# Optimization experiments

Measured on AMD Instinct MI355X. Metric: run time of the kernel, lower is better.

Reference implementation:

```python
import jax, jax.numpy as jnp
import numpy as np

DIM = 768
NH = 12
HD = DIM // NH  # 64, also the depthwise-pool channel count
SR = 2
EPS_SRN = 1e-6   # sr_norm / up_norm eps
EPS_LN = 1e-5    # default nn.LayerNorm eps for norm_q/k/v


def ln(x, g, b, eps):
    m = x.mean(-1, keepdims=True)
    v = x.var(-1, keepdims=True)
    return (x - m) / jnp.sqrt(v + eps) * g + b


def dwconv(x, w, stride, pad, bias=None):
    # x [N,C,H,W], w [C*m,1,kh,kw] (torch depthwise layout), groups = C
    y = jax.lax.conv_general_dilated(
        x, w, (stride, stride), [(pad, pad), (pad, pad)],
        feature_group_count=x.shape[1],
        dimension_numbers=('NCHW', 'OIHW', 'NCHW'))
    return y if bias is None else y + bias[None, :, None, None]


def setup_inputs() -> dict:
    key = jax.random.key(0)
    ks = jax.random.split(key, 8)
    B, H, W = 8, 56, 56
    N = H * W
    s = 0.02
    f32 = jnp.float32
    d = {
        'x': jax.random.normal(ks[0], (B, N, DIM), f32),
        'q_w': jax.random.normal(ks[1], (DIM, DIM), f32) * s,
        'q_b': jnp.zeros((DIM,), f32),
        'kv_w': jax.random.normal(ks[2], (DIM, 2 * DIM), f32) * s,
        'kv_b': jnp.zeros((2 * DIM,), f32),
        'sr_w': jax.random.normal(ks[3], (DIM, 1, 3, 3), f32) * s,
        'sr_b': jnp.zeros((DIM,), f32),
        'srn_g': jnp.ones((DIM,), f32), 'srn_b': jnp.zeros((DIM,), f32),
        'up_w': jax.random.normal(ks[4], (SR * SR * DIM, 1, 3, 3), f32) * s,
        'up_b': jnp.zeros((SR * SR * DIM,), f32),
        'upn_g': jnp.ones((DIM,), f32), 'upn_b': jnp.zeros((DIM,), f32),
        'proj_w': jax.random.normal(ks[5], (DIM, DIM), f32) * s,
        'proj_b': jnp.zeros((DIM,), f32),
        'pq_w': jax.random.normal(ks[6], (HD, 1, 3, 3), f32) * s,
        'pk_w': jax.random.normal(ks[7], (HD, 1, 3, 3), f32) * s,
        'pv_w': jax.random.normal(jax.random.fold_in(key, 7), (HD, 1, 3, 3), f32) * s,
        'nq_g': jnp.ones((HD,), f32), 'nq_b': jnp.zeros((HD,), f32),
        'nk_g': jnp.ones((HD,), f32), 'nk_b': jnp.zeros((HD,), f32),
        'nv_g': jnp.ones((HD,), f32), 'nv_b': jnp.zeros((HD,), f32),
        'H': H, 'W': W,
    }
    return d


def _forward(x, q_w, q_b, kv_w, kv_b, sr_w, sr_b, srn_g, srn_b,
             up_w, up_b, upn_g, upn_b, proj_w, proj_b,
             pq_w, pk_w, pv_w, nq_g, nq_b, nk_g, nk_b, nv_g, nv_b, H, W):
    B, N, C = x.shape
    scale = HD ** -0.5
    # q projection -> [B, NH, N, HD]
    q = (x @ q_w + q_b).reshape(B, N, NH, HD).transpose(0, 2, 1, 3)
    # pool_q: per-head depthwise 3x3 stride-1 conv + LayerNorm(HD)
    qi = q.reshape(B * NH, H, W, HD).transpose(0, 3, 1, 2)
    qi = dwconv(qi, pq_w, 1, 1)
    q = qi.reshape(B, NH, HD, H * W).transpose(0, 1, 3, 2)
    q = ln(q, nq_g, nq_b, EPS_LN)
    # spatial reduction of x (depthwise k=3, s=2, p=1) + LayerNorm
    xs = x.transpose(0, 2, 1).reshape(B, C, H, W)
    xs = dwconv(xs, sr_w, SR, SR // 2, sr_b)
    Hs, Ws = xs.shape[2], xs.shape[3]  # H//SR, W//SR
    xs = xs.reshape(B, C, Hs * Ws).transpose(0, 2, 1)
    xs = ln(xs, srn_g, srn_b, EPS_SRN)
    # kv projection -> k, v [B, NH, Hs*Ws, HD]
    kv = (xs @ kv_w + kv_b).reshape(B, Hs * Ws, 2, NH, HD).transpose(2, 0, 3, 1, 4)
    k, v = kv[0], kv[1]

    def pool_kv(t, w, g, b):
        ti = t.reshape(B * NH, Hs, Ws, HD).transpose(0, 3, 1, 2)
        ti = dwconv(ti, w, 2, 1)  # stride_kv=(2,2), pad 1
        hk, wk = ti.shape[2], ti.shape[3]
        t2 = ti.reshape(B, NH, HD, hk * wk).transpose(0, 1, 3, 2)
        return ln(t2, g, b, EPS_LN)

    kp = pool_kv(k, pk_w, nk_g, nk_b)
    vp = pool_kv(v, pv_w, nv_g, nv_b)
    # attention core
    attn = jax.nn.softmax(jnp.einsum('bhnd,bhmd->bhnm', q, kp) * scale, axis=-1)
    out = jnp.einsum('bhnm,bhmd->bhnd', attn, vp).transpose(0, 2, 1, 3).reshape(B, N, C)
    # identity path: unpooled v -> depthwise conv -> PixelShuffle(SR) upsample
    idn = v.transpose(0, 1, 3, 2).reshape(B, C, Hs, Ws)
    idn = dwconv(idn, up_w, 1, 1, up_b)  # [B, SR*SR*C, Hs, Ws], groups=C
    idn = idn.reshape(B, C, SR, SR, Hs, Ws).transpose(0, 1, 4, 2, 5, 3).reshape(B, C, Hs * SR, Ws * SR)
    idn = idn.reshape(B, C, N).transpose(0, 2, 1)
    idn = ln(idn, upn_g, upn_b, EPS_SRN)
    return (out + idn) @ proj_w + proj_b


def reference(x, q_w, q_b, kv_w, kv_b, sr_w, sr_b, srn_g, srn_b,
              up_w, up_b, upn_g, upn_b, proj_w, proj_b,
              pq_w, pk_w, pv_w, nq_g, nq_b, nk_g, nk_b, nv_g, nv_b, H, W):
    return _forward(x, q_w, q_b, kv_w, kv_b, sr_w, sr_b, srn_g, srn_b,
                    up_w, up_b, upn_g, upn_b, proj_w, proj_b,
                    pq_w, pk_w, pv_w, nq_g, nq_b, nk_g, nk_b, nv_g, nv_b, H, W)
```

## Files before the change

### kernel.cpp

```cpp
#include <hip/hip_runtime.h>
#include <cstdint>
#include <cstddef>

#define DIM 768
#define NHD 12
#define HD  64
#define HH  56
#define WW  56
#define NQ  3136
#define HS  28
#define WSS 28
#define NS  784
#define HK  14
#define WK  14
#define NKK 196
#define NKP 224
#define VSTR 256
#define PROWB 512

typedef __bf16 bf16x8 __attribute__((ext_vector_type(8)));
typedef __bf16 bf16x4 __attribute__((ext_vector_type(4)));
typedef float  f32x4  __attribute__((ext_vector_type(4)));

__device__ __forceinline__ int xcd_swizzle(int bid, int nwg) {
  const int q = nwg >> 3, r = nwg & 7;
  const int xcd = bid & 7, off = bid >> 3;
  return (xcd < r ? xcd * (q + 1) : r * (q + 1) + (xcd - r) * q) + off;
}

__device__ __forceinline__ void gload_lds16(const void* g, void* l) {
  __builtin_amdgcn_global_load_lds(
      (const __attribute__((address_space(1))) void*)g,
      (__attribute__((address_space(3))) void*)l, 16, 0, 0);
}

#define LDP 48

template<int MODE>
__global__ __launch_bounds__(256) void gemm_mfma_kernel(
    const __bf16* __restrict__ A, const __bf16* __restrict__ Bt,
    const float* __restrict__ bias, float* __restrict__ C,
    __bf16* __restrict__ Cq, int M, int N, int K)
{
  __shared__ __bf16 As[128 * LDP];
  __shared__ __bf16 Bs[128 * LDP];

  const int nX = N >> 7;
  const int bid = xcd_swizzle(blockIdx.x, (M >> 7) * nX);
  const int row0 = (bid / nX) << 7;
  const int col0 = (bid % nX) << 7;

  const int t = threadIdx.x;
  const int lane = t & 63;
  const int w = t >> 6;
  const int wr = w >> 1, wc = w & 1;

  const int rs = t >> 1;
  const int kh = (t & 1) << 4;
  const __bf16* Aptr = A + (size_t)(row0 + rs) * K + kh;
  const __bf16* Bptr = Bt + (size_t)(col0 + rs) * K + kh;

  f32x4 acc[4][4];
#pragma unroll
  for (int i = 0; i < 4; ++i)
#pragma unroll
    for (int j = 0; j < 4; ++j) acc[i][j] = (f32x4){0.f, 0.f, 0.f, 0.f};

  const int fr = lane & 15;
  const int fc = lane >> 4;

  int4 a0 = *(const int4*)(Aptr);
  int4 a1 = *(const int4*)(Aptr + 8);
  int4 b0 = *(const int4*)(Bptr);
  int4 b1 = *(const int4*)(Bptr + 8);

  const int NT = K >> 5;
  for (int kt = 0; kt < NT; ++kt) {
    __syncthreads();
    *(int4*)(&As[rs * LDP + kh]) = a0;
    *(int4*)(&As[rs * LDP + kh + 8]) = a1;
    *(int4*)(&Bs[rs * LDP + kh]) = b0;
    *(int4*)(&Bs[rs * LDP + kh + 8]) = b1;
    __syncthreads();
    if (kt + 1 < NT) {
      const __bf16* ap = Aptr + ((kt + 1) << 5);
      const __bf16* bp = Bptr + ((kt + 1) << 5);
      a0 = *(const int4*)(ap);
      a1 = *(const int4*)(ap + 8);
      b0 = *(const int4*)(bp);
      b1 = *(const int4*)(bp + 8);
    }
    bf16x8 af[4], bfr[4];
#pragma unroll
    for (int i = 0; i < 4; ++i)
      af[i] = *(const bf16x8*)(&As[(wr * 64 + i * 16 + fr) * LDP + fc * 8]);
#pragma unroll
    for (int j = 0; j < 4; ++j)
      bfr[j] = *(const bf16x8*)(&Bs[(wc * 64 + j * 16 + fr) * LDP + fc * 8]);
#pragma unroll
    for (int i = 0; i < 4; ++i)
#pragma unroll
      for (int j = 0; j < 4; ++j)
        acc[i][j] = __builtin_amdgcn_mfma_f32_16x16x32_bf16(af[i], bfr[j], acc[i][j], 0, 0, 0);
  }

  const int orow = row0 + wr * 64 + ((lane >> 4) << 2);
  const int ocol = col0 + wc * 64 + (lane & 15);
#pragma unroll
  for (int j = 0; j < 4; ++j) {
    const int col = ocol + j * 16;
    const float bv = bias[col];
#pragma unroll
    for (int i = 0; i < 4; ++i)
#pragma unroll
      for (int r = 0; r < 4; ++r) {
        const int rrow = orow + i * 16 + r;
        if (MODE == 0) {
          C[(size_t)rrow * N + col] = acc[i][j][r] + bv;
        } else if (MODE == 1) {
          const int b = rrow / NQ, n = rrow - b * NQ;
          const int h = col >> 6, hd = col & 63;
          Cq[(((size_t)b * NHD + h) * NQ + n) * HD + hd] = (__bf16)(acc[i][j][r] + bv);
        } else {
          Cq[(size_t)rrow * N + col] = (__bf16)(acc[i][j][r] + bv);
        }
      }
  }
}

__global__ __launch_bounds__(256) void cast_bf16_kernel(
    const float* __restrict__ in, __bf16* __restrict__ out, long n4)
{
  long i = (long)blockIdx.x * 256 + threadIdx.x;
  const long stride = (long)gridDim.x * 256;
  for (; i < n4; i += stride) {
    float4 v = *(const float4*)(in + i * 4);
    bf16x4 o;
    o.x = (__bf16)v.x; o.y = (__bf16)v.y; o.z = (__bf16)v.z; o.w = (__bf16)v.w;
    *(bf16x4*)(out + i * 4) = o;
  }
}

__global__ __launch_bounds__(256) void wt_cast_kernel(
    const float* __restrict__ W, __bf16* __restrict__ Wt, int K, int N)
{
  __shared__ float tile[32][33];
  const int k0 = blockIdx.y << 5;
  const int n0 = blockIdx.x << 5;
  const int tc = threadIdx.x & 31;
  const int tr = threadIdx.x >> 5;
#pragma unroll
  for (int i = 0; i < 4; ++i)
    tile[tr + i * 8][tc] = W[(size_t)(k0 + tr + i * 8) * N + n0 + tc];
  __syncthreads();
#pragma unroll
  for (int i = 0; i < 4; ++i)
    Wt[(size_t)(n0 + tr + i * 8) * K + k0 + tc] = (__bf16)tile[tc][tr + i * 8];
}

__global__ __launch_bounds__(256) void up_tr_kernel(
    const float* __restrict__ upw, float* __restrict__ upt)
{
  const int i = blockIdx.x * 256 + threadIdx.x;
  if (i < 4 * 9 * DIM) {
    const int c = i % DIM;
    const int rest = i / DIM;
    const int tap = rest % 9, sidx = rest / 9;
    upt[i] = upw[(c * 4 + sidx) * 9 + tap];
  }
}

__global__ __launch_bounds__(256) void sr_tr_kernel(
    const float* __restrict__ srw, float* __restrict__ srt)
{
  const int i = blockIdx.x * 256 + threadIdx.x;
  if (i < 9 * DIM) {
    const int c = i % DIM;
    const int tap = i / DIM;
    srt[i] = srw[c * 9 + tap];
  }
}

__global__ __launch_bounds__(256) void pool_q_ln_kernel(
    const __bf16* __restrict__ qp, const float* __restrict__ pqw,
    const float* __restrict__ g, const float* __restrict__ bb,
    __bf16* __restrict__ qf)
{
  const int blk = xcd_swizzle(blockIdx.x, gridDim.x);
  const int bh = blk / HH, y = blk - bh * HH;
  const int lane = threadIdx.x & 63;
  const int w = threadIdx.x >> 6;
  const int x0 = w * (WW / 4);

  float wt[9];
#pragma unroll
  for (int tap = 0; tap < 9; ++tap) {
    const int yy = y - 1 + tap / 3;
    wt[tap] = (yy >= 0 && yy < HH) ? pqw[lane * 9 + tap] : 0.f;
  }
  const float gl = g[lane], bl = bb[lane];

  const __bf16* rp0;
  const __bf16* rp1;
  const __bf16* rp2;
  {
    const __bf16* base = qp + (size_t)bh * NQ * HD + lane;
    rp0 = base + (size_t)min(max(y - 1, 0), HH - 1) * WW * HD;
    rp1 = base + (size_t)y * WW * HD;
    rp2 = base + (size_t)min(max(y + 1, 0), HH - 1) * WW * HD;
  }
  auto ldc = [&](int xx, float* d) {
    const float m = (xx >= 0 && xx < WW) ? 1.f : 0.f;
    const int xc = min(max(xx, 0), WW - 1);
    d[0] = m * (float)rp0[(size_t)xc * HD];
    d[1] = m * (float)rp1[(size_t)xc * HD];
    d[2] = m * (float)rp2[(size_t)xc * HD];
  };

  float c0[3], c1[3], c2[3], cn[3];
  ldc(x0 - 1, c0);
  ldc(x0,     c1);
  ldc(x0 + 1, c2);

#pragma unroll
  for (int xi = 0; xi < WW / 4; ++xi) {
    const int x = x0 + xi;
    ldc(x + 2, cn);
    float acc = 0.f;
#pragma unroll
    for (int dy = 0; dy < 3; ++dy) {
      acc = fmaf(wt[dy * 3 + 0], c0[dy], acc);
      acc = fmaf(wt[dy * 3 + 1], c1[dy], acc);
      acc = fmaf(wt[dy * 3 + 2], c2[dy], acc);
    }
    float s = acc, sq = acc * acc;
#pragma unroll
    for (int off = 32; off > 0; off >>= 1) {
      s  += __shfl_xor(s, off);
      sq += __shfl_xor(sq, off);
    }
    const float mean = s * (1.f / 64.f);
    const float var  = sq * (1.f / 64.f) - mean * mean;
    const float rstd = rsqrtf(var + 1e-5f);
    qf[((size_t)bh * NQ + y * WW + x) * HD + lane] =
        (__bf16)((acc - mean) * rstd * gl + bl);
#pragma unroll
    for (int dy = 0; dy < 3; ++dy) {
      c0[dy] = c1[dy]; c1[dy] = c2[dy]; c2[dy] = cn[dy];
    }
  }
}

__global__ __launch_bounds__(256) void sr_ln_kernel(
    const __bf16* __restrict__ x, const float* __restrict__ srt,
    const float* __restrict__ srb, const float* __restrict__ g,
    const float* __restrict__ bb, __bf16* __restrict__ out)
{
  const int row = xcd_swizzle(blockIdx.x, gridDim.x);
  const int b = row / NS, ns = row - b * NS;
  const int ys = ns / WSS, xs = ns - ys * WSS;
  const int t = threadIdx.x;

  float fm[9];
  size_t off9[9];
#pragma unroll
  for (int tap = 0; tap < 9; ++tap) {
    const int yy = 2 * ys - 1 + tap / 3;
    const int xx = 2 * xs - 1 + tap % 3;
    fm[tap] = (yy >= 0 && yy < HH && xx >= 0 && xx < WW) ? 1.f : 0.f;
    const int yyc = min(max(yy, 0), HH - 1);
    const int xxc = min(max(xx, 0), WW - 1);
    off9[tap] = ((size_t)b * NQ + yyc * WW + xxc) * DIM;
  }

  float vals[3];
  float lsum = 0.f, lsq = 0.f;
#pragma unroll
  for (int i = 0; i < 3; ++i) {
    const int c = t + i * 256;
    float v9[9];
#pragma unroll
    for (int tap = 0; tap < 9; ++tap) v9[tap] = (float)x[off9[tap] + c];
    float acc = srb[c];
#pragma unroll
    for (int tap = 0; tap < 9; ++tap)
      acc = fmaf(srt[tap * DIM + c] * fm[tap], v9[tap], acc);
    vals[i] = acc;
    lsum += acc;
    lsq = fmaf(acc, acc, lsq);
  }
#pragma unroll
  for (int off = 32; off > 0; off >>= 1) {
    lsum += __shfl_xor(lsum, off);
    lsq  += __shfl_xor(lsq, off);
  }
  __shared__ float s1[4], s2[4];
  if ((t & 63) == 0) { s1[t >> 6] = lsum; s2[t >> 6] = lsq; }
  __syncthreads();
  const float S  = s1[0] + s1[1] + s1[2] + s1[3];
  const float SQ = s2[0] + s2[1] + s2[2] + s2[3];
  const float mean = S * (1.f / 768.f);
  const float var  = SQ * (1.f / 768.f) - mean * mean;
  const float rstd = rsqrtf(var + 1e-6f);
#pragma unroll
  for (int i = 0; i < 3; ++i) {
    const int c = t + i * 256;
    out[(size_t)row * DIM + c] = (__bf16)((vals[i] - mean) * rstd * g[c] + bb[c]);
  }
}

__global__ __launch_bounds__(256) void pool_kv_ln_kernel(
    const __bf16* __restrict__ kv, const float* __restrict__ pkw,
    const float* __restrict__ pvw, const float* __restrict__ kg,
    const float* __restrict__ kbb, const float* __restrict__ vg,
    const float* __restrict__ vbb, __bf16* __restrict__ kpb,
    __bf16* __restrict__ vtb)
{
  const int isv = blockIdx.y;
  const float* pw = isv ? pvw : pkw;
  const float* g  = isv ? vg  : kg;
  const float* bb = isv ? vbb : kbb;
  const int coloff = isv ? DIM : 0;

  const int lane = threadIdx.x & 63;
  const int r = blockIdx.x * 4 + (threadIdx.x >> 6);
  const int bh = r / NKP;
  const int nk = r - bh * NKP;

  float val = 0.f;
  if (nk < NKK) {
    const int b = bh / NHD, h = bh - b * NHD;
    const int yk = nk / WK, xk = nk - yk * WK;
    float acc = 0.f;
#pragma unroll
    for (int dy = 0; dy < 3; ++dy) {
      const int yy = 2 * yk - 1 + dy;
      if (yy < 0 || yy >= HS) continue;
#pragma unroll
      for (int dx = 0; dx < 3; ++dx) {
        const int xx = 2 * xk - 1 + dx;
        if (xx < 0 || xx >= WSS) continue;
        acc = fmaf(pw[lane * 9 + dy * 3 + dx],
                   (float)kv[((size_t)b * NS + yy * WSS + xx) * (2 * DIM) + coloff + h * HD + lane], acc);
      }
    }
    float s = acc, sq = acc * acc;
#pragma unroll
    for (int off = 32; off > 0; off >>= 1) {
      s  += __shfl_xor(s, off);
      sq += __shfl_xor(sq, off);
    }
    const float mean = s * (1.f / 64.f);
    const float var  = sq * (1.f / 64.f) - mean * mean;
    const float rstd = rsqrtf(var + 1e-5f);
    val = (acc - mean) * rstd * g[lane] + bb[lane];
  }
  if (!isv) {
    kpb[(size_t)bh * NKP * HD + nk * HD + (lane ^ ((nk & 7) << 3))] = (__bf16)val;
  } else {
    vtb[(size_t)bh * HD * VSTR + lane * VSTR + (nk ^ ((lane & 7) << 3))] = (__bf16)val;
  }
}

__global__ __launch_bounds__(256) void attn_mfma_kernel(
    const __bf16* __restrict__ qf, const __bf16* __restrict__ kpb,
    const __bf16* __restrict__ vtb, __bf16* __restrict__ out)
{
  __shared__ __bf16 kp_lds[16384];
  __shared__ __bf16 v_lds[16384];
  const int bh = blockIdx.y;
  const int qt = blockIdx.x;
  const int t = threadIdx.x;
  const int lane = t & 63, w = t >> 6;
  const int fr = lane & 15;
  const int fg = lane >> 4;
  const int q0 = qt * 64 + w * 16;
  const int sw = (fr & 7) << 4;

  const __bf16* qbase = qf + ((size_t)bh * NQ + q0) * HD;
  const bf16x8 aq0 = *(const bf16x8*)(qbase + fr * HD + fg * 8);
  const bf16x8 aq1 = *(const bf16x8*)(qbase + fr * HD + 32 + fg * 8);

  {
    const __bf16* kgp = kpb + (size_t)bh * (NKP * HD);
    const __bf16* vgp = vtb + (size_t)bh * (HD * VSTR);
    char* kl = (char*)kp_lds;
    char* vl = (char*)v_lds;
#pragma unroll
    for (int i = 0; i < 7; ++i)
      gload_lds16(kgp + (i * 256 + w * 64 + lane) * 8, kl + i * 4096 + w * 1024);
#pragma unroll
    for (int i = 0; i < 8; ++i)
      gload_lds16(vgp + (i * 256 + w * 64 + lane) * 8, vl + i * 4096 + w * 1024);
  }
  __syncthreads();

  const char* kl = (const char*)kp_lds;
  f32x4 s[13];
#pragma unroll
  for (int n = 0; n < 13; ++n) {
    const int rowb = (n * 16 + fr) << 7;
    const bf16x8 b0 = *(const bf16x8*)(kl + rowb + ((fg << 4) ^ sw));
    const bf16x8 b1 = *(const bf16x8*)(kl + rowb + (((fg << 4) + 64) ^ sw));
    f32x4 c = (f32x4){0.f, 0.f, 0.f, 0.f};
    c = __builtin_amdgcn_mfma_f32_16x16x32_bf16(b0, aq0, c, 0, 0, 0);
    c = __builtin_amdgcn_mfma_f32_16x16x32_bf16(b1, aq1, c, 0, 0, 0);
    s[n] = c;
  }
  __syncthreads();

  const float scale = 0.125f;
  char* pb = (char*)kp_lds;
  const int rbase = (w * 16 + fr) * PROWB;
  float sum = 0.f;
#pragma unroll
  for (int n = 0; n < 13; ++n) {
    float e0 = __expf(s[n][0] * scale);
    float e1 = __expf(s[n][1] * scale);
    float e2 = __expf(s[n][2] * scale);
    float e3 = __expf(s[n][3] * scale);
    if (n == 12 && fg >= 1) { e0 = e1 = e2 = e3 = 0.f; }
    sum += (e0 + e1) + (e2 + e3);
    bf16x4 pk4;
    pk4[0] = (__bf16)e0; pk4[1] = (__bf16)e1;
    pk4[2] = (__bf16)e2; pk4[3] = (__bf16)e3;
    *(bf16x4*)(pb + rbase + ((n * 32 + fg * 8) ^ sw)) = pk4;
  }
  {
    bf16x4 z; z[0] = z[1] = z[2] = z[3] = (__bf16)0.f;
    *(bf16x4*)(pb + rbase + ((13 * 32 + fg * 8) ^ sw)) = z;
  }
  sum += __shfl_xor(sum, 16);
  sum += __shfl_xor(sum, 32);
  const float pinvL = 1.f / sum;

  f32x4 acc2[4];
#pragma unroll
  for (int dt = 0; dt < 4; ++dt) acc2[dt] = (f32x4){0.f, 0.f, 0.f, 0.f};
  const char* vl = (const char*)v_lds;
#pragma unroll
  for (int ks = 0; ks < 7; ++ks) {
    const bf16x8 pabf = *(const bf16x8*)(pb + (w * 16 + fr) * PROWB + ((ks * 64 + (fg << 4)) ^ sw));
#pragma unroll
    for (int dt = 0; dt < 4; ++dt) {
      const bf16x8 bv = *(const bf16x8*)(vl + (dt * 16 + fr) * (VSTR * 2) + ((ks * 64 + (fg << 4)) ^ sw));
      acc2[dt] = __builtin_amdgcn_mfma_f32_16x16x32_bf16(pabf, bv, acc2[dt], 0, 0, 0);
    }
  }

  float pr[4];
#pragma unroll
  for (int r = 0; r < 4; ++r)
    pr[r] = __shfl(pinvL, (fg << 4) | (fg * 4 + r));
  const int b = bh / NHD, h = bh - b * NHD;
#pragma unroll
  for (int dt = 0; dt < 4; ++dt)
#pragma unroll
    for (int r = 0; r < 4; ++r)
      out[((size_t)b * NQ + q0 + 4 * fg + r) * DIM + h * HD + dt * 16 + fr] =
          (__bf16)(acc2[dt][r] * pr[r]);
}

#define XCH 2

__global__ __launch_bounds__(256) void idn_add_ln_kernel(
    const __bf16* __restrict__ kv, const float* __restrict__ upt,
    const float* __restrict__ upb, const float* __restrict__ g,
    const float* __restrict__ bb, const __bf16* __restrict__ io,
    __bf16* __restrict__ pj)
{
  int idx = xcd_swizzle(blockIdx.x, gridDim.x);
  const int chunk = idx & (XCH - 1); idx >>= 1;
  const int ys = idx % HS; idx /= HS;
  const int sidx = idx & 3;
  const int b = idx >> 2;
  const int sy = sidx >> 1, sx = sidx & 1;
  const int y = 2 * ys + sy;
  const int t = threadIdx.x;
  const int w = t >> 6;

  float wreg[3][9], ubias[3], gg[3], gb[3];
#pragma unroll
  for (int i = 0; i < 3; ++i) {
    const int c = t + i * 256;
    ubias[i] = upb[c * 4 + sidx];
    gg[i] = g[c];
    gb[i] = bb[c];
#pragma unroll
    for (int tap = 0; tap < 9; ++tap) {
      const int yy = ys - 1 + tap / 3;
      const float f = (yy >= 0 && yy < HS) ? 1.f : 0.f;
      wreg[i][tap] = upt[(sidx * 9 + tap) * DIM + c] * f;
    }
  }

  __shared__ __bf16 vals_lds[14][DIM];
  __shared__ float s1[14][4], s2[14][4];
  const int xs0 = chunk * 14;

  const int y0 = max(ys - 1, 0), y1 = ys, y2 = min(ys + 1, HS - 1);
  const __bf16* vb0 = kv + ((size_t)(b * NS + y0 * WSS)) * (2 * DIM) + DIM + t;
  const __bf16* vb1 = kv + ((size_t)(b * NS + y1 * WSS)) * (2 * DIM) + DIM + t;
  const __bf16* vb2 = kv + ((size_t)(b * NS + y2 * WSS)) * (2 * DIM) + DIM + t;

  auto ldcol = [&](int ch, int p, float* dst) {
    const float m = (p >= 0 && p < WSS) ? 1.f : 0.f;
    const int xx = min(max(p, 0), WSS - 1);
    const size_t off = (size_t)xx * (2 * DIM) + ch * 256;
    dst[0] = m * (float)vb0[off];
    dst[1] = m * (float)vb1[off];
    dst[2] = m * (float)vb2[off];
  };

  float c0[3][3], c1[3][3], c2[3][3], cn[3][3];
#pragma unroll
  for (int ch = 0; ch < 3; ++ch) {
    ldcol(ch, xs0 - 1, c0[ch]);
    ldcol(ch, xs0,     c1[ch]);
    ldcol(ch, xs0 + 1, c2[ch]);
  }

#pragma unroll
  for (int xi = 0; xi < 14; ++xi) {
    const int xs = xs0 + xi;
#pragma unroll
    for (int ch = 0; ch < 3; ++ch) ldcol(ch, xs + 2, cn[ch]);
    float lsum = 0.f, lsq = 0.f;
#pragma unroll
    for (int ch = 0; ch < 3; ++ch) {
      float acc = ubias[ch];
#pragma unroll
      for (int dy = 0; dy < 3; ++dy) {
        acc = fmaf(wreg[ch][dy * 3 + 0], c0[ch][dy], acc);
        acc = fmaf(wreg[ch][dy * 3 + 1], c1[ch][dy], acc);
        acc = fmaf(wreg[ch][dy * 3 + 2], c2[ch][dy], acc);
      }
      vals_lds[xi][t + ch * 256] = (__bf16)acc;
      lsum += acc;
      lsq = fmaf(acc, acc, lsq);
    }
#pragma unroll
    for (int off = 32; off > 0; off >>= 1) {
      lsum += __shfl_xor(lsum, off);
      lsq  += __shfl_xor(lsq, off);
    }
    if ((t & 63) == 0) { s1[xi][w] = lsum; s2[xi][w] = lsq; }
#pragma unroll
    for (int ch = 0; ch < 3; ++ch)
#pragma unroll
      for (int dy = 0; dy < 3; ++dy) {
        c0[ch][dy] = c1[ch][dy];
        c1[ch][dy] = c2[ch][dy];
        c2[ch][dy] = cn[ch][dy];
      }
  }
  __syncthreads();

#pragma unroll
  for (int xi = 0; xi < 14; ++xi) {
    const float S  = s1[xi][0] + s1[xi][1] + s1[xi][2] + s1[xi][3];
    const float SQ = s2[xi][0] + s2[xi][1] + s2[xi][2] + s2[xi][3];
    const float mean = S * (1.f / 768.f);
    const float var  = SQ * (1.f / 768.f) - mean * mean;
    const float rstd = rsqrtf(var + 1e-6f);
    const int x = 2 * (xs0 + xi) + sx;
    const size_t row = (size_t)b * NQ + y * WW + x;
#pragma unroll
    for (int ch = 0; ch < 3; ++ch) {
      const int c = t + ch * 256;
      pj[row * DIM + c] =
          (__bf16)((float)io[row * DIM + c] +
                   ((float)vals_lds[xi][c] - mean) * rstd * gg[ch] + gb[ch]);
    }
  }
}

extern "C" void kernel_launch(void* const* d_in, const int* in_sizes, int n_in,
                              void* d_out, int out_size, void* d_ws, size_t ws_size,
                              hipStream_t stream)
{
  const float* x      = (const float*)d_in[0];
  const float* q_w    = (const float*)d_in[1];
  const float* q_b    = (const float*)d_in[2];
  const float* kv_w   = (const float*)d_in[3];
  const float* kv_b   = (const float*)d_in[4];
  const float* sr_w   = (const float*)d_in[5];
  const float* sr_b   = (const float*)d_in[6];
  const float* srn_g  = (const float*)d_in[7];
  const float* srn_b  = (const float*)d_in[8];
  const float* up_w   = (const float*)d_in[9];
  const float* up_b   = (const float*)d_in[10];
  const float* upn_g  = (const float*)d_in[11];
  const float* upn_b  = (const float*)d_in[12];
  const float* proj_w = (const float*)d_in[13];
  const float* proj_b = (const float*)d_in[14];
  const float* pq_w   = (const float*)d_in[15];
  const float* pk_w   = (const float*)d_in[16];
  const float* pv_w   = (const float*)d_in[17];
  const float* nq_g   = (const float*)d_in[18];
  const float* nq_b   = (const float*)d_in[19];
  const float* nk_g   = (const float*)d_in[20];
  const float* nk_b   = (const float*)d_in[21];
  const float* nv_g   = (const float*)d_in[22];
  const float* nv_b   = (const float*)d_in[23];

  const int B = in_sizes[0] / (NQ * DIM);
  const int M1 = B * NQ;
  const int M2 = B * NS;

  char* p = (char*)d_ws;
  __bf16* xb    = (__bf16*)p;  p += (size_t)M1 * DIM * 2;
  float*  qproj = (float*)p;   p += (size_t)M1 * DIM * 4;
  __bf16* qf    = (__bf16*)p;  p += (size_t)M1 * DIM * 2;
  __bf16* xsln  = (__bf16*)p;  p += (size_t)M2 * DIM * 2;
  __bf16* kvb   = (__bf16*)p;  p += (size_t)M2 * 2 * DIM * 2;
  __bf16* kpb   = (__bf16*)p;  p += (size_t)B * NHD * NKP * HD * 2;
  __bf16* vtb   = (__bf16*)p;  p += (size_t)B * NHD * HD * VSTR * 2;
  __bf16* wqt   = (__bf16*)p;  p += (size_t)DIM * DIM * 2;
  __bf16* wkvt  = (__bf16*)p;  p += (size_t)DIM * 2 * DIM * 2;
  __bf16* wpjt  = (__bf16*)p;  p += (size_t)DIM * DIM * 2;
  float*  upt   = (float*)p;   p += (size_t)4 * 9 * DIM * 4;
  float*  srt   = (float*)p;   p += (size_t)9 * DIM * 4;
  __bf16* qp      = (__bf16*)qproj;
  __bf16* attnout = (__bf16*)qproj;
  __bf16* pjin    = xb;

  dim3 blk(256);

  cast_bf16_kernel<<<2048, blk, 0, stream>>>(x, xb, (long)M1 * DIM / 4);
  wt_cast_kernel<<<dim3(DIM / 32, DIM / 32), blk, 0, stream>>>(q_w, wqt, DIM, DIM);
  wt_cast_kernel<<<dim3(2 * DIM / 32, DIM / 32), blk, 0, stream>>>(kv_w, wkvt, DIM, 2 * DIM);
  wt_cast_kernel<<<dim3(DIM / 32, DIM / 32), blk, 0, stream>>>(proj_w, wpjt, DIM, DIM);
  up_tr_kernel<<<(4 * 9 * DIM + 255) / 256, blk, 0, stream>>>(up_w, upt);
  sr_tr_kernel<<<(9 * DIM + 255) / 256, blk, 0, stream>>>(sr_w, srt);

  gemm_mfma_kernel<1><<<(M1 / 128) * (DIM / 128), blk, 0, stream>>>(
      xb, wqt, q_b, nullptr, qp, M1, DIM, DIM);

  pool_q_ln_kernel<<<B * NHD * HH, blk, 0, stream>>>(
      qp, pq_w, nq_g, nq_b, qf);

  sr_ln_kernel<<<B * NS, blk, 0, stream>>>(
      xb, srt, sr_b, srn_g, srn_b, xsln);

  gemm_mfma_kernel<2><<<(M2 / 128) * (2 * DIM / 128), blk, 0, stream>>>(
      xsln, wkvt, kv_b, nullptr, kvb, M2, 2 * DIM, DIM);

  pool_kv_ln_kernel<<<dim3((B * NHD * NKP) / 4, 2), blk, 0, stream>>>(
      kvb, pk_w, pv_w, nk_g, nk_b, nv_g, nv_b, kpb, vtb);

  attn_mfma_kernel<<<dim3(NQ / 64, B * NHD), blk, 0, stream>>>(
      qf, kpb, vtb, attnout);

  idn_add_ln_kernel<<<B * 4 * HS * XCH, blk, 0, stream>>>(
      kvb, upt, up_b, upn_g, upn_b, attnout, pjin);

  gemm_mfma_kernel<0><<<(M1 / 128) * (DIM / 128), blk, 0, stream>>>(
      pjin, wpjt, proj_b, (float*)d_out, nullptr, M1, DIM, DIM);
}
```

Baseline: 327.9 us.

## Keep softmax probabilities in registers via shuffles and share one LDS buffer for K/V

```diff
diff --git a/kernel.cpp b/kernel.cpp
--- a/kernel.cpp
+++ b/kernel.cpp
@@ -16,7 +16,6 @@
 #define NKK 196
 #define NKP 224
 #define VSTR 256
-#define PROWB 512
 
 typedef __bf16 bf16x8 __attribute__((ext_vector_type(8)));
 typedef __bf16 bf16x4 __attribute__((ext_vector_type(4)));
@@ -34,7 +33,13 @@
       (__attribute__((address_space(3))) void*)l, 16, 0, 0);
 }
 
-#define LDP 48
+__device__ __forceinline__ unsigned pack_bf2(float a, float b) {
+  union { __bf16 h; unsigned short u; } lo, hi;
+  lo.h = (__bf16)a; hi.h = (__bf16)b;
+  return (unsigned)lo.u | ((unsigned)hi.u << 16);
+}
+
+#define LDP 40
 
 template<int MODE>
 __global__ __launch_bounds__(256) void gemm_mfma_kernel(
@@ -366,8 +371,7 @@
     const __bf16* __restrict__ qf, const __bf16* __restrict__ kpb,
     const __bf16* __restrict__ vtb, __bf16* __restrict__ out)
 {
-  __shared__ __bf16 kp_lds[16384];
-  __shared__ __bf16 v_lds[16384];
+  __shared__ __bf16 kv_lds[16384];
   const int bh = blockIdx.y;
   const int qt = blockIdx.x;
   const int t = threadIdx.x;
@@ -381,21 +385,15 @@
   const bf16x8 aq0 = *(const bf16x8*)(qbase + fr * HD + fg * 8);
   const bf16x8 aq1 = *(const bf16x8*)(qbase + fr * HD + 32 + fg * 8);
 
+  char* kl = (char*)kv_lds;
   {
     const __bf16* kgp = kpb + (size_t)bh * (NKP * HD);
-    const __bf16* vgp = vtb + (size_t)bh * (HD * VSTR);
-    char* kl = (char*)kp_lds;
-    char* vl = (char*)v_lds;
 #pragma unroll
     for (int i = 0; i < 7; ++i)
       gload_lds16(kgp + (i * 256 + w * 64 + lane) * 8, kl + i * 4096 + w * 1024);
-#pragma unroll
-    for (int i = 0; i < 8; ++i)
-      gload_lds16(vgp + (i * 256 + w * 64 + lane) * 8, vl + i * 4096 + w * 1024);
   }
   __syncthreads();
 
-  const char* kl = (const char*)kp_lds;
   f32x4 s[13];
 #pragma unroll
   for (int n = 0; n < 13; ++n) {
@@ -409,9 +407,15 @@
   }
   __syncthreads();
 
+  {
+    const __bf16* vgp = vtb + (size_t)bh * (HD * VSTR);
+#pragma unroll
+    for (int i = 0; i < 8; ++i)
+      gload_lds16(vgp + (i * 256 + w * 64 + lane) * 8, kl + i * 4096 + w * 1024);
+  }
+
   const float scale = 0.125f;
-  char* pb = (char*)kp_lds;
-  const int rbase = (w * 16 + fr) * PROWB;
+  unsigned pk[28];
   float sum = 0.f;
 #pragma unroll
   for (int n = 0; n < 13; ++n) {
@@ -421,26 +425,35 @@
     float e3 = __expf(s[n][3] * scale);
     if (n == 12 && fg >= 1) { e0 = e1 = e2 = e3 = 0.f; }
     sum += (e0 + e1) + (e2 + e3);
-    bf16x4 pk4;
-    pk4[0] = (__bf16)e0; pk4[1] = (__bf16)e1;
-    pk4[2] = (__bf16)e2; pk4[3] = (__bf16)e3;
-    *(bf16x4*)(pb + rbase + ((n * 32 + fg * 8) ^ sw)) = pk4;
-  }
-  {
-    bf16x4 z; z[0] = z[1] = z[2] = z[3] = (__bf16)0.f;
-    *(bf16x4*)(pb + rbase + ((13 * 32 + fg * 8) ^ sw)) = z;
-  }
+    pk[2 * n]     = pack_bf2(e0, e1);
+    pk[2 * n + 1] = pack_bf2(e2, e3);
+  }
+  pk[26] = 0u; pk[27] = 0u;
   sum += __shfl_xor(sum, 16);
   sum += __shfl_xor(sum, 32);
   const float pinvL = 1.f / sum;
 
+  __syncthreads();
+
+  const int L1 = ((fg & 1) << 5) | fr;
+  const int L2 = L1 + 16;
+  const bool hi = (fg >= 2);
   f32x4 acc2[4];
 #pragma unroll
   for (int dt = 0; dt < 4; ++dt) acc2[dt] = (f32x4){0.f, 0.f, 0.f, 0.f};
-  const char* vl = (const char*)v_lds;
+  const char* vl = (const char*)kv_lds;
 #pragma unroll
   for (int ks = 0; ks < 7; ++ks) {
-    const bf16x8 pabf = *(const bf16x8*)(pb + (w * 16 + fr) * PROWB + ((ks * 64 + (fg << 4)) ^ sw));
+    const unsigned d0a = __shfl(pk[4 * ks + 0], L1), d0b = __shfl(pk[4 * ks + 2], L1);
+    const unsigned d1a = __shfl(pk[4 * ks + 1], L1), d1b = __shfl(pk[4 * ks + 3], L1);
+    const unsigned d2a = __shfl(pk[4 * ks + 0], L2), d2b = __shfl(pk[4 * ks + 2], L2);
+    const unsigned d3a = __shfl(pk[4 * ks + 1], L2), d3b = __shfl(pk[4 * ks + 3], L2);
+    uint4 pu;
+    pu.x = hi ? d0b : d0a;
+    pu.y = hi ? d1b : d1a;
+    pu.z = hi ? d2b : d2a;
+    pu.w = hi ? d3b : d3a;
+    const bf16x8 pabf = __builtin_bit_cast(bf16x8, pu);
 #pragma unroll
     for (int dt = 0; dt < 4; ++dt) {
       const bf16x8 bv = *(const bf16x8*)(vl + (dt * 16 + fr) * (VSTR * 2) + ((ks * 64 + (fg << 4)) ^ sw));
```

New measurement: 329.3 us. About the same (+0.4%).
